# Optimization experiments

Measured on AMD Instinct MI355X. Metric: run time of the kernel, lower is better.

## Reference

```python
import jax, jax.numpy as jnp
import numpy as np
import math

IN_F, OUT_F, GRID = 1024, 1024, 7
BATCH, SEQ = 4, 4096


def _l2norm(v, eps=1e-12):
    return v / (jnp.linalg.norm(v) + eps)


def setup_inputs() -> dict:
    key = jax.random.key(0)
    k0, k1, k2, k3 = jax.random.split(key, 4)
    x = jax.random.normal(k0, (BATCH, SEQ, IN_F), dtype=jnp.float32)
    # spectral-normed base linear (weights nonzero for a meaningful baseline)
    base_w = jax.random.normal(k1, (OUT_F, IN_F), dtype=jnp.float32) * 0.02
    base_b = jnp.zeros((OUT_F,), dtype=jnp.float32)
    u = jax.random.normal(k2, (OUT_F,), dtype=jnp.float32)  # power-iteration buffer
    # Chebyshev translation points and fixed logspace scales (as in __init__)
    steps = jnp.arange(GRID, dtype=jnp.float32)
    translation = (-jnp.cos((2.0 * steps + 1.0) / (2.0 * GRID) * math.pi) * 1.5).reshape(1, 1, GRID)
    scale = (1.0 * jnp.logspace(-0.5, 0.5, GRID)).reshape(1, 1, GRID).astype(jnp.float32)
    wavelet_w = jax.random.normal(k3, (OUT_F, IN_F * GRID), dtype=jnp.float32) * 0.01
    soft_threshold = jnp.array([0.005], dtype=jnp.float32)
    output_scale = jnp.array([1.0], dtype=jnp.float32)
    return dict(x=x, base_w=base_w, base_b=base_b, u=u, translation=translation,
                scale=scale, wavelet_w=wavelet_w, soft_threshold=soft_threshold,
                output_scale=output_scale)


def reference(x, base_w, base_b, u, translation, scale, wavelet_w, soft_threshold, output_scale):
    x_flat = x.reshape(-1, x.shape[-1])  # [N, IN]
    # spectral norm: one power iteration (no grad through u, v), sigma = u' W v
    v = jax.lax.stop_gradient(_l2norm(base_w.T @ u))
    u2 = jax.lax.stop_gradient(_l2norm(base_w @ v))
    sigma = u2 @ (base_w @ v)
    w_sn = base_w / sigma
    base_out = jax.nn.silu(x_flat) @ w_sn.T + base_b  # [N, OUT]
    # wavelet (Ricker) basis expansion
    safe_scale = jnp.maximum(jnp.abs(scale), 0.1)  # [1,1,G]
    x_norm = jnp.tanh(x_flat) * 2.5  # [N, IN]
    xe = (x_norm[:, :, None] - translation) / safe_scale  # [N, IN, G]
    basis = (1.0 - xe * xe) * jnp.exp(-0.5 * xe * xe)
    kan = basis.reshape(x_flat.shape[0], -1) @ wavelet_w.T  # [N, OUT]
    thr = jax.nn.softplus(soft_threshold)
    kan = jnp.sign(kan) * jax.nn.relu(jnp.abs(kan) - thr)
    out = (base_out + kan) * output_scale
    return out.reshape(*x.shape[:-1], wavelet_w.shape[0])
```

## Files before the change

kernel.cpp:

```cpp
#include <hip/hip_runtime.h>
#include <math.h>


typedef __attribute__((ext_vector_type(4))) float  f32x4;
typedef __attribute__((ext_vector_type(8))) __bf16 bf16x8;
typedef __attribute__((ext_vector_type(8))) unsigned short u16x8;

#define NROWS 16384
#define INF   1024
#define OUTF  1024
#define GG    7
#define KKAN  7168
#define KTOT  8192

static __device__ __forceinline__ unsigned short f2bf(float f) {
  union { float f; unsigned int u; } v; v.f = f;
  unsigned int r = v.u + 0x7fffu + ((v.u >> 16) & 1u);
  return (unsigned short)(r >> 16);
}

__global__ void zero_t(float* __restrict__ t) { t[threadIdx.x] = 0.f; }

__global__ void wtu_acc(const float* __restrict__ W, const float* __restrict__ u,
                        float* __restrict__ t) {
  int tid = threadIdx.x;
  int j4 = tid * 4;
  int i0 = blockIdx.x * 16;
  f32x4 acc = {0.f, 0.f, 0.f, 0.f};
  for (int i = i0; i < i0 + 16; ++i) {
    float ui = u[i];
    f32x4 w4 = *(const f32x4*)(W + (size_t)i * INF + j4);
    acc[0] += w4[0] * ui; acc[1] += w4[1] * ui;
    acc[2] += w4[2] * ui; acc[3] += w4[3] * ui;
  }
  atomicAdd(&t[j4 + 0], acc[0]);
  atomicAdd(&t[j4 + 1], acc[1]);
  atomicAdd(&t[j4 + 2], acc[2]);
  atomicAdd(&t[j4 + 3], acc[3]);
}

__global__ void mv_w_t(const float* __restrict__ W, const float* __restrict__ t,
                       float* __restrict__ s) {
  int i = blockIdx.x;
  int tid = threadIdx.x;
  float p = 0.f;
  for (int j = tid; j < INF; j += 256) p += W[(size_t)i * INF + j] * t[j];
  __shared__ float red[256];
  red[tid] = p; __syncthreads();
  for (int k = 128; k > 0; k >>= 1) { if (tid < k) red[tid] += red[tid + k]; __syncthreads(); }
  if (tid == 0) s[i] = red[0];
}

__global__ void sigma_finish(const float* __restrict__ t, const float* __restrict__ s,
                             const float* __restrict__ st, const float* __restrict__ os,
                             float* __restrict__ scal) {
  __shared__ float r1[256], r2[256];
  int tid = threadIdx.x;
  float p1 = 0.f, p2 = 0.f;
  for (int i = tid; i < 1024; i += 256) { float a = t[i]; p1 += a * a; float b = s[i]; p2 += b * b; }
  r1[tid] = p1; r2[tid] = p2; __syncthreads();
  for (int k = 128; k > 0; k >>= 1) { if (tid < k) { r1[tid] += r1[tid + k]; r2[tid] += r2[tid + k]; } __syncthreads(); }
  if (tid == 0) {
    float nt = sqrtf(r1[0]);
    float ns = sqrtf(r2[0]);
    float nq = ns / (nt + 1e-12f);
    float sigma = nq * nq / (nq + 1e-12f);
    scal[0] = 1.f / sigma;
    scal[1] = log1pf(__expf(st[0]));
    scal[2] = os[0];
  }
}

__global__ void wsn_cast(const float* __restrict__ w, const float* __restrict__ scal,
                         unsigned short* __restrict__ Wp) {
  float is = scal[0];
  int idx = blockIdx.x * 256 + threadIdx.x;
  int row = idx >> 7, i0 = (idx & 127) << 3;
  const f32x4* p = (const f32x4*)(w + (size_t)row * INF + i0);
  f32x4 a = p[0], b = p[1];
  u16x8 v;
  v[0] = f2bf(a[0] * is); v[1] = f2bf(a[1] * is); v[2] = f2bf(a[2] * is); v[3] = f2bf(a[3] * is);
  v[4] = f2bf(b[0] * is); v[5] = f2bf(b[1] * is); v[6] = f2bf(b[2] * is); v[7] = f2bf(b[3] * is);
  *(u16x8*)(Wp + (size_t)row * KTOT + KKAN + i0) = v;
}

__global__ void wkan_cast(const float* __restrict__ w, unsigned short* __restrict__ Wp) {
  __shared__ float row[KKAN];
  int orow = blockIdx.x;
  const float* src = w + (size_t)orow * KKAN;
  for (int c = threadIdx.x * 4; c < KKAN; c += 1024)
    *(f32x4*)&row[c] = *(const f32x4*)&src[c];
  __syncthreads();
  unsigned short* dst = Wp + (size_t)orow * KTOT;
  for (int r = threadIdx.x; r < 896; r += 256) {
    int g = r >> 7, i0 = (r & 127) << 3;
    u16x8 v;
#pragma unroll
    for (int j = 0; j < 8; j++) v[j] = f2bf(row[(i0 + j) * GG + g]);
    *(u16x8*)(dst + g * 1024 + i0) = v;
  }
}

__global__ void expand_kernel(const float* __restrict__ x,
                              const float* __restrict__ translation,
                              const float* __restrict__ scale,
                              unsigned short* __restrict__ Ap,
                              int row0, int nrows) {
  float tr[GG], iss[GG];
#pragma unroll
  for (int g = 0; g < GG; g++) {
    tr[g] = translation[g];
    float s = fabsf(scale[g]);
    iss[g] = 1.f / (s < 0.1f ? 0.1f : s);
  }
  int units = nrows * (INF / 8);
  int stride = gridDim.x * blockDim.x;
  for (int uu = blockIdx.x * blockDim.x + threadIdx.x; uu < units; uu += stride) {
    int nloc = uu >> 7;
    int i0 = (uu & 127) << 3;
    const f32x4* xp = (const f32x4*)(x + (size_t)(row0 + nloc) * INF + i0);
    f32x4 xa = xp[0], xb = xp[1];
    float xv[8] = {xa[0], xa[1], xa[2], xa[3], xb[0], xb[1], xb[2], xb[3]};
    u16x8 sb, kb[GG];
#pragma unroll
    for (int j = 0; j < 8; j++) {
      float xx = xv[j];
      float si = xx / (1.f + __expf(-xx));
      sb[j] = f2bf(si);
      float e2 = __expf(2.f * xx);
      float xn = 2.5f * (1.f - 2.f / (e2 + 1.f));
#pragma unroll
      for (int g = 0; g < GG; g++) {
        float xe = (xn - tr[g]) * iss[g];
        float t2 = xe * xe;
        float b = (1.f - t2) * __expf(-0.5f * t2);
        kb[g][j] = f2bf(b);
      }
    }
    unsigned short* rp = Ap + (size_t)nloc * KTOT;
    *(u16x8*)(rp + KKAN + i0) = sb;
#pragma unroll
    for (int g = 0; g < GG; g++) *(u16x8*)(rp + g * 1024 + i0) = kb[g];
  }
}

static __device__ __forceinline__ void gload16(const unsigned short* g, unsigned short* l) {
  __builtin_amdgcn_global_load_lds(
      (const __attribute__((address_space(1))) unsigned int*)g,
      (__attribute__((address_space(3))) unsigned int*)l, 16, 0, 0);
}

#define SCB   __builtin_amdgcn_sched_barrier(0)
#define SBAR  do { SCB; __builtin_amdgcn_s_barrier(); } while (0)
#define VM(N) asm volatile("s_waitcnt vmcnt(" #N ")" ::: "memory")
#define LG(N) asm volatile("s_waitcnt lgkmcnt(" #N ")" ::: "memory")

#define STAGE(db, tt) do { \
    const unsigned short* _sa = gA + (size_t)(tt) * 64; \
    const unsigned short* _sb = gB + (size_t)(tt) * 64; \
    unsigned short* _da = ldsS + (db) * 24576; \
    unsigned short* _db = ldsS + (db) * 24576 + 16384; \
    gload16(_sa,                       _da); \
    gload16(_sa + (size_t)64  * KTOT,  _da + 4096); \
    gload16(_sa + (size_t)128 * KTOT,  _da + 8192); \
    gload16(_sa + (size_t)192 * KTOT,  _da + 12288); \
    gload16(_sb,                       _db); \
    gload16(_sb + (size_t)64  * KTOT,  _db + 4096); \
  } while (0)

#define RD8(FA, FB, bb, kx) do { \
    _Pragma("unroll") for (int i = 0; i < 4; ++i) \
      FA[i] = *(const bf16x8*)(pA + (bb) * 49152 + i * 2048 + (kx)); \
    _Pragma("unroll") for (int j = 0; j < 4; ++j) \
      FB[j] = *(const bf16x8*)(pB + (bb) * 49152 + j * 2048 + (kx)); \
  } while (0)

#define MM16(FA, FB) do { _Pragma("unroll") for (int i = 0; i < 4; ++i) \
    _Pragma("unroll") for (int j = 0; j < 4; ++j) \
      acc[i][j] = __builtin_amdgcn_mfma_f32_16x16x32_bf16(FA[i], FB[j], acc[i][j], 0, 0, 0); } while (0)

#define TILE(tt, bb, nb, db, SS, NR, W1) do { \
    RD8(fYA, fYB, bb, kx1); \
    SCB; \
    if (SS) STAGE(db, (tt) + 2); \
    SCB; \
    __builtin_amdgcn_s_setprio(1); MM16(fXA, fXB); __builtin_amdgcn_s_setprio(0); \
    LG(0); SCB; \
    W1; \
    SBAR; \
    if (NR) { RD8(fXA, fXB, nb, kx0); SCB; } \
    __builtin_amdgcn_s_setprio(1); MM16(fYA, fYB); __builtin_amdgcn_s_setprio(0); \
    LG(0); SCB; \
  } while (0)

__global__ __launch_bounds__(512, 2) void gemm_k(
    const unsigned short* __restrict__ A,
    const unsigned short* __restrict__ W,
    const float* __restrict__ bias,
    const float* __restrict__ scal,
    float* __restrict__ out) {
  __shared__ unsigned short lds[73728];

  int bid = blockIdx.x;
  int cpx = gridDim.x >> 3;
  int swz = (bid & 7) * cpx + (bid >> 3);
  int m0 = (swz >> 3) * 256;
  int n0 = (swz & 7) * 128;
  int tid = threadIdx.x;
  int wv = tid >> 6, l = tid & 63;
  int wr = wv >> 1, wc = wv & 1;

  float thr = scal[1], osc = scal[2];

  int rowq = tid >> 3;
  int swk = ((tid & 7) ^ (rowq & 7)) << 3;
  const unsigned short* gA = A + (size_t)(m0 + rowq) * KTOT + swk;
  const unsigned short* gB = W + (size_t)(n0 + rowq) * KTOT + swk;
  unsigned short* ldsS = lds + wv * 512;

  int lr = l & 15;
  int kb = (l >> 4) << 4;
  int xr = (l & 7) << 4;
  int kx0 = kb ^ xr;
  int kx1 = (64 | kb) ^ xr;
  const char* pA = (const char*)lds + (wr * 64 + lr) * 128;
  const char* pB = (const char*)lds + 32768 + (wc * 64 + lr) * 128;

  bf16x8 fXA[4], fXB[4], fYA[4], fYB[4];
  f32x4 acc[4][4] = {};

  STAGE(0, 0);
  STAGE(1, 1);
  VM(6);
  SBAR;
  RD8(fXA, fXB, 0, kx0);
  LG(0); SCB;

  for (int t = 0; t < 108; t += 3) {
    TILE(t,     0, 1, 2, 1, 1, VM(6));
    TILE(t + 1, 1, 2, 0, 1, 1, VM(6));
    TILE(t + 2, 2, 0, 1, 1, 1, VM(6));
  }
  TILE(108, 0, 1, 2, 1, 1, VM(6));
  TILE(109, 1, 2, 0, 1, 1, VM(6));
  TILE(110, 2, 0, 1, 1, 1, VM(6));
  TILE(111, 0, 1, 2, 1, 1, VM(6));

#pragma unroll
  for (int i = 0; i < 4; ++i)
#pragma unroll
    for (int j = 0; j < 4; ++j)
#pragma unroll
      for (int e = 0; e < 4; ++e) {
        float v = acc[i][j][e];
        float a = fabsf(v) - thr;
        a = a > 0.f ? a : 0.f;
        acc[i][j][e] = v > 0.f ? a : -a;
      }

  for (int t = 112; t < 124; t += 3) {
    TILE(t,     1, 2, 0, 1, 1, VM(6));
    TILE(t + 1, 2, 0, 1, 1, 1, VM(6));
    TILE(t + 2, 0, 1, 2, 1, 1, VM(6));
  }
  TILE(124, 1, 2, 0, 1, 1, VM(6));
  TILE(125, 2, 0, 1, 1, 1, VM(6));
  TILE(126, 0, 1, 2, 0, 1, VM(0));
  TILE(127, 1, 2, 0, 0, 0, (void)0);

  int rr = m0 + wr * 64 + ((l >> 4) << 2);
  int cc = n0 + wc * 64 + lr;
#pragma unroll
  for (int i = 0; i < 4; ++i)
#pragma unroll
    for (int j = 0; j < 4; ++j) {
      int c = cc + j * 16;
      float bc = bias[c];
#pragma unroll
      for (int e = 0; e < 4; ++e) {
        int r = rr + i * 16 + e;
        out[(size_t)r * OUTF + c] = (acc[i][j][e] + bc) * osc;
      }
    }
}

extern "C" void kernel_launch(void* const* d_in, const int* in_sizes, int n_in,
                              void* d_out, int out_size, void* d_ws, size_t ws_size,
                              hipStream_t stream) {
  const float* x              = (const float*)d_in[0];
  const float* base_w         = (const float*)d_in[1];
  const float* base_b         = (const float*)d_in[2];
  const float* u              = (const float*)d_in[3];
  const float* translation    = (const float*)d_in[4];
  const float* scale          = (const float*)d_in[5];
  const float* wavelet_w      = (const float*)d_in[6];
  const float* soft_threshold = (const float*)d_in[7];
  const float* output_scale   = (const float*)d_in[8];
  float* out = (float*)d_out;

  char* ws = (char*)d_ws;
  float* t_vec = (float*)ws;
  float* s_vec = t_vec + 1024;
  float* scal  = s_vec + 1024;
  unsigned short* Wp = (unsigned short*)(ws + 16384);
  char* dynbuf = ws + 16384 + (size_t)KTOT * OUTF * 2;

  size_t fixed = 16384 + (size_t)KTOT * OUTF * 2;
  size_t avail = ws_size > fixed ? ws_size - fixed : 0;

  zero_t<<<1, 1024, 0, stream>>>(t_vec);
  wtu_acc<<<64, 256, 0, stream>>>(base_w, u, t_vec);
  mv_w_t<<<1024, 256, 0, stream>>>(base_w, t_vec, s_vec);
  sigma_finish<<<1, 256, 0, stream>>>(t_vec, s_vec, soft_threshold, output_scale, scal);
  wsn_cast<<<512, 256, 0, stream>>>(base_w, scal, Wp);
  wkan_cast<<<1024, 256, 0, stream>>>(wavelet_w, Wp);

  const size_t ROW = (size_t)KTOT * 2;
  size_t total = (size_t)NROWS * ROW;
  int nch = (int)((total + (avail > 0 ? avail : 1) - 1) / (avail > 0 ? avail : 1));
  if (nch < 1) nch = 1;
  long mc = (((NROWS + nch - 1) / nch) + 255) & ~255L;
  while (mc > 256 && (size_t)mc * ROW > avail) mc -= 256;
  if (mc < 256) mc = 256;

  unsigned short* Ap = (unsigned short*)dynbuf;

  for (long r0 = 0; r0 < NROWS; r0 += mc) {
    long nr = (NROWS - r0 < mc) ? (NROWS - r0) : mc;
    expand_kernel<<<2048, 256, 0, stream>>>(x, translation, scale, Ap, (int)r0, (int)nr);
    int mt = (int)(nr / 256);
    gemm_k<<<mt * 8, 512, 0, stream>>>(Ap, Wp, base_b, scal, out + (size_t)r0 * OUTF);
  }
}
```

Before: 334.1 us.

## Deepen GEMM prefetch to three tiles and read full K-tile fragments at once

Restructures the bf16 MFMA main loop so each tile loads both K-halves of its A/B fragments from LDS in one pass and runs 32 MFMAs per tile instead of two 16-MFMA half-steps. Global staging now runs three tiles ahead across the three LDS buffers, with one barrier per tile instead of per half-step. The aim is fewer barriers and more slack to hide global-load latency. In exchange, the fragment register sets double in size, which under the 512-thread, 2-blocks-per-CU launch bound risks register spills or scheduling stalls.

New measurement: 336.9 us. Within noise of the previous version (+0.8%).

```diff
diff --git a/kernel.cpp b/kernel.cpp
--- a/kernel.cpp
+++ b/kernel.cpp
@@ -168,30 +168,39 @@
     gload16(_sb + (size_t)64  * KTOT,  _db + 4096); \
   } while (0)
 
-#define RD8(FA, FB, bb, kx) do { \
+#define RD16(FA, FB, bb) do { \
+    _Pragma("unroll") for (int i = 0; i < 4; ++i) { \
+      FA[i]     = *(const bf16x8*)(pA + (bb) * 49152 + i * 2048 + kx0); \
+      FA[4 + i] = *(const bf16x8*)(pA + (bb) * 49152 + i * 2048 + kx1); \
+    } \
+    _Pragma("unroll") for (int j = 0; j < 4; ++j) { \
+      FB[j]     = *(const bf16x8*)(pB + (bb) * 49152 + j * 2048 + kx0); \
+      FB[4 + j] = *(const bf16x8*)(pB + (bb) * 49152 + j * 2048 + kx1); \
+    } \
+  } while (0)
+
+#define MM32(FA, FB) do { \
     _Pragma("unroll") for (int i = 0; i < 4; ++i) \
-      FA[i] = *(const bf16x8*)(pA + (bb) * 49152 + i * 2048 + (kx)); \
     _Pragma("unroll") for (int j = 0; j < 4; ++j) \
-      FB[j] = *(const bf16x8*)(pB + (bb) * 49152 + j * 2048 + (kx)); \
+      acc[i][j] = __builtin_amdgcn_mfma_f32_16x16x32_bf16(FA[i], FB[j], acc[i][j], 0, 0, 0); \
+    _Pragma("unroll") for (int i = 0; i < 4; ++i) \
+    _Pragma("unroll") for (int j = 0; j < 4; ++j) \
+      acc[i][j] = __builtin_amdgcn_mfma_f32_16x16x32_bf16(FA[4 + i], FB[4 + j], acc[i][j], 0, 0, 0); \
   } while (0)
 
-#define MM16(FA, FB) do { _Pragma("unroll") for (int i = 0; i < 4; ++i) \
-    _Pragma("unroll") for (int j = 0; j < 4; ++j) \
-      acc[i][j] = __builtin_amdgcn_mfma_f32_16x16x32_bf16(FA[i], FB[j], acc[i][j], 0, 0, 0); } while (0)
-
-#define TILE(tt, bb, nb, db, SS, NR, W1) do { \
-    RD8(fYA, fYB, bb, kx1); \
+#define TILE(tt, rb, sb, SS, RA, RB, MA, MB, WAIT) do { \
+    RD16(RA, RB, rb); \
     SCB; \
-    if (SS) STAGE(db, (tt) + 2); \
+    if (SS) STAGE(sb, (tt) + 3); \
     SCB; \
-    __builtin_amdgcn_s_setprio(1); MM16(fXA, fXB); __builtin_amdgcn_s_setprio(0); \
+    __builtin_amdgcn_s_setprio(1); MM32(MA, MB); __builtin_amdgcn_s_setprio(0); \
     LG(0); SCB; \
-    W1; \
+    WAIT; \
     SBAR; \
-    if (NR) { RD8(fXA, fXB, nb, kx0); SCB; } \
-    __builtin_amdgcn_s_setprio(1); MM16(fYA, fYB); __builtin_amdgcn_s_setprio(0); \
-    LG(0); SCB; \
   } while (0)
+
+#define TILEX(tt, rb, sb, SS, WAIT) TILE(tt, rb, sb, SS, fYA, fYB, fXA, fXB, WAIT)
+#define TILEY(tt, rb, sb, SS, WAIT) TILE(tt, rb, sb, SS, fXA, fXB, fYA, fYB, WAIT)
 
 __global__ __launch_bounds__(512, 2) void gemm_k(
     const unsigned short* __restrict__ A,
@@ -226,25 +235,30 @@
   const char* pA = (const char*)lds + (wr * 64 + lr) * 128;
   const char* pB = (const char*)lds + 32768 + (wc * 64 + lr) * 128;
 
-  bf16x8 fXA[4], fXB[4], fYA[4], fYB[4];
+  bf16x8 fXA[8], fXB[8], fYA[8], fYB[8];
   f32x4 acc[4][4] = {};
 
   STAGE(0, 0);
   STAGE(1, 1);
+  STAGE(2, 2);
   VM(6);
   SBAR;
-  RD8(fXA, fXB, 0, kx0);
+  RD16(fXA, fXB, 0);
   LG(0); SCB;
-
-  for (int t = 0; t < 108; t += 3) {
-    TILE(t,     0, 1, 2, 1, 1, VM(6));
-    TILE(t + 1, 1, 2, 0, 1, 1, VM(6));
-    TILE(t + 2, 2, 0, 1, 1, 1, VM(6));
-  }
-  TILE(108, 0, 1, 2, 1, 1, VM(6));
-  TILE(109, 1, 2, 0, 1, 1, VM(6));
-  TILE(110, 2, 0, 1, 1, 1, VM(6));
-  TILE(111, 0, 1, 2, 1, 1, VM(6));
+  SBAR;
+
+  for (int t = 0; t < 108; t += 6) {
+    TILEX(t,     1, 0, 1, VM(6));
+    TILEY(t + 1, 2, 1, 1, VM(6));
+    TILEX(t + 2, 0, 2, 1, VM(6));
+    TILEY(t + 3, 1, 0, 1, VM(6));
+    TILEX(t + 4, 2, 1, 1, VM(6));
+    TILEY(t + 5, 0, 2, 1, VM(6));
+  }
+  TILEX(108, 1, 0, 1, VM(6));
+  TILEY(109, 2, 1, 1, VM(6));
+  TILEX(110, 0, 2, 1, VM(6));
+  TILEY(111, 1, 0, 1, VM(6));
 
 #pragma unroll
   for (int i = 0; i < 4; ++i)
@@ -258,15 +272,22 @@
         acc[i][j][e] = v > 0.f ? a : -a;
       }
 
-  for (int t = 112; t < 124; t += 3) {
-    TILE(t,     1, 2, 0, 1, 1, VM(6));
-    TILE(t + 1, 2, 0, 1, 1, 1, VM(6));
-    TILE(t + 2, 0, 1, 2, 1, 1, VM(6));
-  }
-  TILE(124, 1, 2, 0, 1, 1, VM(6));
-  TILE(125, 2, 0, 1, 1, 1, VM(6));
-  TILE(126, 0, 1, 2, 0, 1, VM(0));
-  TILE(127, 1, 2, 0, 0, 0, (void)0);
+  TILEX(112, 2, 1, 1, VM(6));
+  TILEY(113, 0, 2, 1, VM(6));
+  TILEX(114, 1, 0, 1, VM(6));
+  TILEY(115, 2, 1, 1, VM(6));
+  TILEX(116, 0, 2, 1, VM(6));
+  TILEY(117, 1, 0, 1, VM(6));
+  TILEX(118, 2, 1, 1, VM(6));
+  TILEY(119, 0, 2, 1, VM(6));
+  TILEX(120, 1, 0, 1, VM(6));
+  TILEY(121, 2, 1, 1, VM(6));
+  TILEX(122, 0, 2, 1, VM(6));
+  TILEY(123, 1, 0, 1, VM(6));
+  TILEX(124, 2, 1, 1, VM(6));
+  TILEY(125, 0, 0, 0, VM(0));
+  TILEX(126, 1, 0, 0, (void)0);
+  __builtin_amdgcn_s_setprio(1); MM32(fYA, fYB); __builtin_amdgcn_s_setprio(0);
 
   int rr = m0 + wr * 64 + ((l >> 4) << 2);
   int cc = n0 + wc * 64 + lr;
```

## Halve GEMM block to 4 waves, each computing a 128x64 output tile

Applied to the files above, without the earlier changes.

The GEMM block keeps its 256x128 output tile but now runs 256 threads (4 waves) instead of 512 (8 waves). Each wave computes a 128x64 sub-tile with 8x4 MFMA accumulators, so each B fragment read from LDS is reused across twice as many MFMAs. Staging loops are rescaled to 8 A-row and 4 B-row global-to-LDS loads per thread, with matching vmcnt waits. The cost is much higher register pressure and only one wave per SIMD, which leaves less room to hide LDS and memory latency.

After: 373.7 us. 1.12x slower.

```diff
diff --git a/kernel.cpp b/kernel.cpp
--- a/kernel.cpp
+++ b/kernel.cpp
@@ -159,41 +159,39 @@
     const unsigned short* _sa = gA + (size_t)(tt) * 64; \
     const unsigned short* _sb = gB + (size_t)(tt) * 64; \
     unsigned short* _da = ldsS + (db) * 24576; \
-    unsigned short* _db = ldsS + (db) * 24576 + 16384; \
-    gload16(_sa,                       _da); \
-    gload16(_sa + (size_t)64  * KTOT,  _da + 4096); \
-    gload16(_sa + (size_t)128 * KTOT,  _da + 8192); \
-    gload16(_sa + (size_t)192 * KTOT,  _da + 12288); \
-    gload16(_sb,                       _db); \
-    gload16(_sb + (size_t)64  * KTOT,  _db + 4096); \
+    unsigned short* _db2 = ldsS + (db) * 24576 + 16384; \
+    _Pragma("unroll") for (int r = 0; r < 8; ++r) \
+      gload16(_sa + (size_t)(r * 32) * KTOT, _da + r * 2048); \
+    _Pragma("unroll") for (int r = 0; r < 4; ++r) \
+      gload16(_sb + (size_t)(r * 32) * KTOT, _db2 + r * 2048); \
   } while (0)
 
-#define RD8(FA, FB, bb, kx) do { \
-    _Pragma("unroll") for (int i = 0; i < 4; ++i) \
+#define RD12(FA, FB, bb, kx) do { \
+    _Pragma("unroll") for (int i = 0; i < 8; ++i) \
       FA[i] = *(const bf16x8*)(pA + (bb) * 49152 + i * 2048 + (kx)); \
     _Pragma("unroll") for (int j = 0; j < 4; ++j) \
       FB[j] = *(const bf16x8*)(pB + (bb) * 49152 + j * 2048 + (kx)); \
   } while (0)
 
-#define MM16(FA, FB) do { _Pragma("unroll") for (int i = 0; i < 4; ++i) \
+#define MM32h(FA, FB) do { _Pragma("unroll") for (int i = 0; i < 8; ++i) \
     _Pragma("unroll") for (int j = 0; j < 4; ++j) \
       acc[i][j] = __builtin_amdgcn_mfma_f32_16x16x32_bf16(FA[i], FB[j], acc[i][j], 0, 0, 0); } while (0)
 
 #define TILE(tt, bb, nb, db, SS, NR, W1) do { \
-    RD8(fYA, fYB, bb, kx1); \
+    RD12(fYA, fYB, bb, kx1); \
     SCB; \
     if (SS) STAGE(db, (tt) + 2); \
     SCB; \
-    __builtin_amdgcn_s_setprio(1); MM16(fXA, fXB); __builtin_amdgcn_s_setprio(0); \
+    __builtin_amdgcn_s_setprio(1); MM32h(fXA, fXB); __builtin_amdgcn_s_setprio(0); \
     LG(0); SCB; \
     W1; \
     SBAR; \
-    if (NR) { RD8(fXA, fXB, nb, kx0); SCB; } \
-    __builtin_amdgcn_s_setprio(1); MM16(fYA, fYB); __builtin_amdgcn_s_setprio(0); \
+    if (NR) { RD12(fXA, fXB, nb, kx0); SCB; } \
+    __builtin_amdgcn_s_setprio(1); MM32h(fYA, fYB); __builtin_amdgcn_s_setprio(0); \
     LG(0); SCB; \
   } while (0)
 
-__global__ __launch_bounds__(512, 2) void gemm_k(
+__global__ __launch_bounds__(256, 1) void gemm_k(
     const unsigned short* __restrict__ A,
     const unsigned short* __restrict__ W,
     const float* __restrict__ bias,
@@ -223,31 +221,31 @@
   int xr = (l & 7) << 4;
   int kx0 = kb ^ xr;
   int kx1 = (64 | kb) ^ xr;
-  const char* pA = (const char*)lds + (wr * 64 + lr) * 128;
+  const char* pA = (const char*)lds + (wr * 128 + lr) * 128;
   const char* pB = (const char*)lds + 32768 + (wc * 64 + lr) * 128;
 
-  bf16x8 fXA[4], fXB[4], fYA[4], fYB[4];
-  f32x4 acc[4][4] = {};
+  bf16x8 fXA[8], fXB[4], fYA[8], fYB[4];
+  f32x4 acc[8][4] = {};
 
   STAGE(0, 0);
   STAGE(1, 1);
-  VM(6);
+  VM(12);
   SBAR;
-  RD8(fXA, fXB, 0, kx0);
+  RD12(fXA, fXB, 0, kx0);
   LG(0); SCB;
 
   for (int t = 0; t < 108; t += 3) {
-    TILE(t,     0, 1, 2, 1, 1, VM(6));
-    TILE(t + 1, 1, 2, 0, 1, 1, VM(6));
-    TILE(t + 2, 2, 0, 1, 1, 1, VM(6));
-  }
-  TILE(108, 0, 1, 2, 1, 1, VM(6));
-  TILE(109, 1, 2, 0, 1, 1, VM(6));
-  TILE(110, 2, 0, 1, 1, 1, VM(6));
-  TILE(111, 0, 1, 2, 1, 1, VM(6));
-
-#pragma unroll
-  for (int i = 0; i < 4; ++i)
+    TILE(t,     0, 1, 2, 1, 1, VM(12));
+    TILE(t + 1, 1, 2, 0, 1, 1, VM(12));
+    TILE(t + 2, 2, 0, 1, 1, 1, VM(12));
+  }
+  TILE(108, 0, 1, 2, 1, 1, VM(12));
+  TILE(109, 1, 2, 0, 1, 1, VM(12));
+  TILE(110, 2, 0, 1, 1, 1, VM(12));
+  TILE(111, 0, 1, 2, 1, 1, VM(12));
+
+#pragma unroll
+  for (int i = 0; i < 8; ++i)
 #pragma unroll
     for (int j = 0; j < 4; ++j)
 #pragma unroll
@@ -258,20 +256,27 @@
         acc[i][j][e] = v > 0.f ? a : -a;
       }
 
-  for (int t = 112; t < 124; t += 3) {
-    TILE(t,     1, 2, 0, 1, 1, VM(6));
-    TILE(t + 1, 2, 0, 1, 1, 1, VM(6));
-    TILE(t + 2, 0, 1, 2, 1, 1, VM(6));
-  }
-  TILE(124, 1, 2, 0, 1, 1, VM(6));
-  TILE(125, 2, 0, 1, 1, 1, VM(6));
+  TILE(112, 1, 2, 0, 1, 1, VM(12));
+  TILE(113, 2, 0, 1, 1, 1, VM(12));
+  TILE(114, 0, 1, 2, 1, 1, VM(12));
+  TILE(115, 1, 2, 0, 1, 1, VM(12));
+  TILE(116, 2, 0, 1, 1, 1, VM(12));
+  TILE(117, 0, 1, 2, 1, 1, VM(12));
+  TILE(118, 1, 2, 0, 1, 1, VM(12));
+  TILE(119, 2, 0, 1, 1, 1, VM(12));
+  TILE(120, 0, 1, 2, 1, 1, VM(12));
+  TILE(121, 1, 2, 0, 1, 1, VM(12));
+  TILE(122, 2, 0, 1, 1, 1, VM(12));
+  TILE(123, 0, 1, 2, 1, 1, VM(12));
+  TILE(124, 1, 2, 0, 1, 1, VM(12));
+  TILE(125, 2, 0, 1, 1, 1, VM(12));
   TILE(126, 0, 1, 2, 0, 1, VM(0));
   TILE(127, 1, 2, 0, 0, 0, (void)0);
 
-  int rr = m0 + wr * 64 + ((l >> 4) << 2);
+  int rr = m0 + wr * 128 + ((l >> 4) << 2);
   int cc = n0 + wc * 64 + lr;
 #pragma unroll
-  for (int i = 0; i < 4; ++i)
+  for (int i = 0; i < 8; ++i)
 #pragma unroll
     for (int j = 0; j < 4; ++j) {
       int c = cc + j * 16;
@@ -329,6 +334,6 @@
     long nr = (NROWS - r0 < mc) ? (NROWS - r0) : mc;
     expand_kernel<<<2048, 256, 0, stream>>>(x, translation, scale, Ap, (int)r0, (int)nr);
     int mt = (int)(nr / 256);
-    gemm_k<<<mt * 8, 512, 0, stream>>>(Ap, Wp, base_b, scal, out + (size_t)r0 * OUTF);
-  }
-}
+    gemm_k<<<mt * 8, 256, 0, stream>>>(Ap, Wp, base_b, scal, out + (size_t)r0 * OUTF);
+  }
+}
```

## Fuse Ricker basis expansion into GEMM A-tile generation

Applied to the files above, without the earlier changes.

Removes the materialized 16384x8192 bf16 expanded activation matrix. A prep kernel now writes only bf16 silu(x) and fp32 tanh-normalized x. The GEMM computes the seven wavelet basis values per K tile in registers and writes them into LDS instead of loading A tiles from global memory. The wavelet weights are reordered into a matching (i-chunk, g) interleaved layout. This trades much HBM traffic for per-tile exp work in the GEMM main loop, which may compete with MFMA issue and raise register pressure.

New measurement: 506.4 us. +51.6%, slower.

```diff
diff --git a/kernel.cpp b/kernel.cpp
--- a/kernel.cpp
+++ b/kernel.cpp
@@ -5,6 +5,7 @@
 typedef __attribute__((ext_vector_type(4))) float  f32x4;
 typedef __attribute__((ext_vector_type(8))) __bf16 bf16x8;
 typedef __attribute__((ext_vector_type(8))) unsigned short u16x8;
+typedef __attribute__((ext_vector_type(4))) unsigned int u32x4;
 
 #define NROWS 16384
 #define INF   1024
@@ -97,31 +98,23 @@
     u16x8 v;
 #pragma unroll
     for (int j = 0; j < 8; j++) v[j] = f2bf(row[(i0 + j) * GG + g]);
-    *(u16x8*)(dst + g * 1024 + i0) = v;
-  }
-}
-
-__global__ void expand_kernel(const float* __restrict__ x,
-                              const float* __restrict__ translation,
-                              const float* __restrict__ scale,
-                              unsigned short* __restrict__ Ap,
-                              int row0, int nrows) {
-  float tr[GG], iss[GG];
-#pragma unroll
-  for (int g = 0; g < GG; g++) {
-    tr[g] = translation[g];
-    float s = fabsf(scale[g]);
-    iss[g] = 1.f / (s < 0.1f ? 0.1f : s);
-  }
-  int units = nrows * (INF / 8);
+    *(u16x8*)(dst + ((i0 >> 6) * 7 + g) * 64 + (i0 & 63)) = v;
+  }
+}
+
+__global__ void xs_prep(const float* __restrict__ x,
+                        unsigned short* __restrict__ siluP,
+                        float* __restrict__ xnP) {
+  int units = NROWS * (INF / 8);
   int stride = gridDim.x * blockDim.x;
   for (int uu = blockIdx.x * blockDim.x + threadIdx.x; uu < units; uu += stride) {
-    int nloc = uu >> 7;
+    int row = uu >> 7;
     int i0 = (uu & 127) << 3;
-    const f32x4* xp = (const f32x4*)(x + (size_t)(row0 + nloc) * INF + i0);
+    const f32x4* xp = (const f32x4*)(x + (size_t)row * INF + i0);
     f32x4 xa = xp[0], xb = xp[1];
     float xv[8] = {xa[0], xa[1], xa[2], xa[3], xb[0], xb[1], xb[2], xb[3]};
-    u16x8 sb, kb[GG];
+    u16x8 sb;
+    f32x4 na, nb;
 #pragma unroll
     for (int j = 0; j < 8; j++) {
       float xx = xv[j];
@@ -129,18 +122,12 @@
       sb[j] = f2bf(si);
       float e2 = __expf(2.f * xx);
       float xn = 2.5f * (1.f - 2.f / (e2 + 1.f));
-#pragma unroll
-      for (int g = 0; g < GG; g++) {
-        float xe = (xn - tr[g]) * iss[g];
-        float t2 = xe * xe;
-        float b = (1.f - t2) * __expf(-0.5f * t2);
-        kb[g][j] = f2bf(b);
-      }
+      if (j < 4) na[j] = xn; else nb[j - 4] = xn;
     }
-    unsigned short* rp = Ap + (size_t)nloc * KTOT;
-    *(u16x8*)(rp + KKAN + i0) = sb;
-#pragma unroll
-    for (int g = 0; g < GG; g++) *(u16x8*)(rp + g * 1024 + i0) = kb[g];
+    *(u16x8*)(siluP + (size_t)row * INF + i0) = sb;
+    float* np = xnP + (size_t)row * INF + i0;
+    *(f32x4*)np = na;
+    *(f32x4*)(np + 4) = nb;
   }
 }
 
@@ -150,22 +137,61 @@
       (__attribute__((address_space(3))) unsigned int*)l, 16, 0, 0);
 }
 
+static __device__ __forceinline__ float basisf(float x, float is_, float ntri) {
+  float xe = fmaf(x, is_, ntri);
+  float t2 = xe * xe;
+  float ex = __expf(-0.5f * t2);
+  return (1.f - t2) * ex;
+}
+
 #define SCB   __builtin_amdgcn_sched_barrier(0)
 #define SBAR  do { SCB; __builtin_amdgcn_s_barrier(); } while (0)
 #define VM(N) asm volatile("s_waitcnt vmcnt(" #N ")" ::: "memory")
 #define LG(N) asm volatile("s_waitcnt lgkmcnt(" #N ")" ::: "memory")
 
-#define STAGE(db, tt) do { \
-    const unsigned short* _sa = gA + (size_t)(tt) * 64; \
-    const unsigned short* _sb = gB + (size_t)(tt) * 64; \
+#define XLOAD(ic) do { \
+    const f32x4* xp_ = (const f32x4*)(xnp + (size_t)(m0 + xrow) * 1024 + (ic) * 64 + 32 * xh); \
+    _Pragma("unroll") for (int q = 0; q < 8; ++q) xd[q] = xp_[q]; \
+  } while (0)
+
+#define BGLOAD(db, t2) do { \
+    const unsigned short* _sb = gB + (size_t)(t2) * 64; \
+    unsigned short* _db2 = ldsS + (db) * 24576 + 16384; \
+    gload16(_sb, _db2); \
+    gload16(_sb + (size_t)64 * KTOT, _db2 + 4096); \
+  } while (0)
+
+#define CW(db, t2) do { \
+    int g2s = (t2) % 7; \
+    float is_ = ldsF[g2s]; \
+    float ntri = ldsF[7 + g2s]; \
+    char* wp_ = (char*)lds + (db) * 49152 + xrow * 128; \
+    _Pragma("unroll") for (int q = 0; q < 4; ++q) { \
+      unsigned int ov0, ov1, ov2, ov3; \
+      { f32x4 xv = xd[2 * q]; \
+        float b0 = basisf(xv[0], is_, ntri), b1 = basisf(xv[1], is_, ntri); \
+        float b2 = basisf(xv[2], is_, ntri), b3 = basisf(xv[3], is_, ntri); \
+        asm("v_cvt_pk_bf16_f32 %0, %1, %2" : "=v"(ov0) : "v"(b0), "v"(b1)); \
+        asm("v_cvt_pk_bf16_f32 %0, %1, %2" : "=v"(ov1) : "v"(b2), "v"(b3)); } \
+      { f32x4 xv = xd[2 * q + 1]; \
+        float b0 = basisf(xv[0], is_, ntri), b1 = basisf(xv[1], is_, ntri); \
+        float b2 = basisf(xv[2], is_, ntri), b3 = basisf(xv[3], is_, ntri); \
+        asm("v_cvt_pk_bf16_f32 %0, %1, %2" : "=v"(ov2) : "v"(b0), "v"(b1)); \
+        asm("v_cvt_pk_bf16_f32 %0, %1, %2" : "=v"(ov3) : "v"(b2), "v"(b3)); } \
+      u32x4 w4 = {ov0, ov1, ov2, ov3}; \
+      *(u32x4*)(wp_ + (((4 * xh + q) ^ (xrow & 7)) << 4)) = w4; \
+    } \
+  } while (0)
+
+#define STAGE_BASE(db, t2) do { \
+    const unsigned short* _sa = gS + (size_t)((t2) - 112) * 64; \
+    const unsigned short* _sb = gB + (size_t)(t2) * 64; \
     unsigned short* _da = ldsS + (db) * 24576; \
-    unsigned short* _db = ldsS + (db) * 24576 + 16384; \
-    gload16(_sa,                       _da); \
-    gload16(_sa + (size_t)64  * KTOT,  _da + 4096); \
-    gload16(_sa + (size_t)128 * KTOT,  _da + 8192); \
-    gload16(_sa + (size_t)192 * KTOT,  _da + 12288); \
-    gload16(_sb,                       _db); \
-    gload16(_sb + (size_t)64  * KTOT,  _db + 4096); \
+    unsigned short* _db2 = _da + 16384; \
+    _Pragma("unroll") for (int r = 0; r < 4; ++r) \
+      gload16(_sa + (size_t)(r * 64) * 1024, _da + r * 4096); \
+    _Pragma("unroll") for (int r = 0; r < 2; ++r) \
+      gload16(_sb + (size_t)(r * 64) * KTOT, _db2 + r * 4096); \
   } while (0)
 
 #define RD8(FA, FB, bb, kx) do { \
@@ -179,10 +205,28 @@
     _Pragma("unroll") for (int j = 0; j < 4; ++j) \
       acc[i][j] = __builtin_amdgcn_mfma_f32_16x16x32_bf16(FA[i], FB[j], acc[i][j], 0, 0, 0); } while (0)
 
-#define TILE(tt, bb, nb, db, SS, NR, W1) do { \
+#define TILE_K(tt, bb, nb, db, W1) do { \
     RD8(fYA, fYB, bb, kx1); \
     SCB; \
-    if (SS) STAGE(db, (tt) + 2); \
+    { int t2_ = (tt) + 2; int g2_ = t2_ % 7; int ic_ = t2_ / 7; \
+      if (g2_ == 0) { XLOAD(ic_); } \
+      SCB; \
+      BGLOAD(db, t2_); \
+      SCB; \
+      __builtin_amdgcn_s_setprio(1); MM16(fXA, fXB); __builtin_amdgcn_s_setprio(0); \
+      CW(db, t2_); } \
+    LG(0); SCB; \
+    W1; \
+    SBAR; \
+    RD8(fXA, fXB, nb, kx0); SCB; \
+    __builtin_amdgcn_s_setprio(1); MM16(fYA, fYB); __builtin_amdgcn_s_setprio(0); \
+    LG(0); SCB; \
+  } while (0)
+
+#define TILE_B(tt, bb, nb, db, SS, NR, W1) do { \
+    RD8(fYA, fYB, bb, kx1); \
+    SCB; \
+    if (SS) STAGE_BASE(db, (tt) + 2); \
     SCB; \
     __builtin_amdgcn_s_setprio(1); MM16(fXA, fXB); __builtin_amdgcn_s_setprio(0); \
     LG(0); SCB; \
@@ -194,12 +238,16 @@
   } while (0)
 
 __global__ __launch_bounds__(512, 2) void gemm_k(
-    const unsigned short* __restrict__ A,
+    const float* __restrict__ xnp,
+    const unsigned short* __restrict__ silu,
     const unsigned short* __restrict__ W,
     const float* __restrict__ bias,
     const float* __restrict__ scal,
+    const float* __restrict__ trP,
+    const float* __restrict__ scP,
     float* __restrict__ out) {
-  __shared__ unsigned short lds[73728];
+  __shared__ unsigned short lds[73760];
+  float* ldsF = (float*)(lds + 73728);
 
   int bid = blockIdx.x;
   int cpx = gridDim.x >> 3;
@@ -214,9 +262,12 @@
 
   int rowq = tid >> 3;
   int swk = ((tid & 7) ^ (rowq & 7)) << 3;
-  const unsigned short* gA = A + (size_t)(m0 + rowq) * KTOT + swk;
   const unsigned short* gB = W + (size_t)(n0 + rowq) * KTOT + swk;
+  const unsigned short* gS = silu + (size_t)(m0 + rowq) * 1024 + swk;
   unsigned short* ldsS = lds + wv * 512;
+
+  int xrow = tid >> 1;
+  int xh = tid & 1;
 
   int lr = l & 15;
   int kb = (l >> 4) << 4;
@@ -227,24 +278,41 @@
   const char* pB = (const char*)lds + 32768 + (wc * 64 + lr) * 128;
 
   bf16x8 fXA[4], fXB[4], fYA[4], fYB[4];
+  f32x4 xd[8];
   f32x4 acc[4][4] = {};
 
-  STAGE(0, 0);
-  STAGE(1, 1);
-  VM(6);
+  if (tid < 7) {
+    float s = fabsf(scP[tid]);
+    s = s < 0.1f ? 0.1f : s;
+    float is_ = 1.0f / s;
+    ldsF[tid] = is_;
+    ldsF[7 + tid] = -trP[tid] * is_;
+  }
+  SBAR;
+
+  XLOAD(0);
+  SCB;
+  BGLOAD(0, 0);
+  SCB;
+  CW(0, 0);
+  BGLOAD(1, 1);
+  SCB;
+  CW(1, 1);
+  LG(0);
+  VM(2);
   SBAR;
   RD8(fXA, fXB, 0, kx0);
   LG(0); SCB;
 
   for (int t = 0; t < 108; t += 3) {
-    TILE(t,     0, 1, 2, 1, 1, VM(6));
-    TILE(t + 1, 1, 2, 0, 1, 1, VM(6));
-    TILE(t + 2, 2, 0, 1, 1, 1, VM(6));
-  }
-  TILE(108, 0, 1, 2, 1, 1, VM(6));
-  TILE(109, 1, 2, 0, 1, 1, VM(6));
-  TILE(110, 2, 0, 1, 1, 1, VM(6));
-  TILE(111, 0, 1, 2, 1, 1, VM(6));
+    TILE_K(t,     0, 1, 2, VM(2));
+    TILE_K(t + 1, 1, 2, 0, VM(2));
+    TILE_K(t + 2, 2, 0, 1, VM(2));
+  }
+  TILE_K(108, 0, 1, 2, VM(2));
+  TILE_K(109, 1, 2, 0, VM(2));
+  TILE_B(110, 2, 0, 1, 1, 1, VM(6));
+  TILE_B(111, 0, 1, 2, 1, 1, VM(6));
 
 #pragma unroll
   for (int i = 0; i < 4; ++i)
@@ -258,15 +326,22 @@
         acc[i][j][e] = v > 0.f ? a : -a;
       }
 
-  for (int t = 112; t < 124; t += 3) {
-    TILE(t,     1, 2, 0, 1, 1, VM(6));
-    TILE(t + 1, 2, 0, 1, 1, 1, VM(6));
-    TILE(t + 2, 0, 1, 2, 1, 1, VM(6));
-  }
-  TILE(124, 1, 2, 0, 1, 1, VM(6));
-  TILE(125, 2, 0, 1, 1, 1, VM(6));
-  TILE(126, 0, 1, 2, 0, 1, VM(0));
-  TILE(127, 1, 2, 0, 0, 0, (void)0);
+  TILE_B(112, 1, 2, 0, 1, 1, VM(6));
+  TILE_B(113, 2, 0, 1, 1, 1, VM(6));
+  TILE_B(114, 0, 1, 2, 1, 1, VM(6));
+  TILE_B(115, 1, 2, 0, 1, 1, VM(6));
+  TILE_B(116, 2, 0, 1, 1, 1, VM(6));
+  TILE_B(117, 0, 1, 2, 1, 1, VM(6));
+  TILE_B(118, 1, 2, 0, 1, 1, VM(6));
+  TILE_B(119, 2, 0, 1, 1, 1, VM(6));
+  TILE_B(120, 0, 1, 2, 1, 1, VM(6));
+  TILE_B(121, 1, 2, 0, 1, 1, VM(6));
+  TILE_B(122, 2, 0, 1, 1, 1, VM(6));
+  TILE_B(123, 0, 1, 2, 1, 1, VM(6));
+  TILE_B(124, 1, 2, 0, 1, 1, VM(6));
+  TILE_B(125, 2, 0, 1, 1, 1, VM(6));
+  TILE_B(126, 0, 1, 2, 0, 1, VM(0));
+  TILE_B(127, 1, 2, 0, 0, 0, (void)0);
 
   int rr = m0 + wr * 64 + ((l >> 4) << 2);
   int cc = n0 + wc * 64 + lr;
@@ -302,11 +377,9 @@
   float* t_vec = (float*)ws;
   float* s_vec = t_vec + 1024;
   float* scal  = s_vec + 1024;
-  unsigned short* Wp = (unsigned short*)(ws + 16384);
-  char* dynbuf = ws + 16384 + (size_t)KTOT * OUTF * 2;
-
-  size_t fixed = 16384 + (size_t)KTOT * OUTF * 2;
-  size_t avail = ws_size > fixed ? ws_size - fixed : 0;
+  unsigned short* Wp    = (unsigned short*)(ws + 16384);
+  unsigned short* siluP = (unsigned short*)(ws + 16384 + (size_t)KTOT * OUTF * 2);
+  float* xnP = (float*)(ws + 16384 + (size_t)KTOT * OUTF * 2 + (size_t)NROWS * INF * 2);
 
   zero_t<<<1, 1024, 0, stream>>>(t_vec);
   wtu_acc<<<64, 256, 0, stream>>>(base_w, u, t_vec);
@@ -314,21 +387,8 @@
   sigma_finish<<<1, 256, 0, stream>>>(t_vec, s_vec, soft_threshold, output_scale, scal);
   wsn_cast<<<512, 256, 0, stream>>>(base_w, scal, Wp);
   wkan_cast<<<1024, 256, 0, stream>>>(wavelet_w, Wp);
-
-  const size_t ROW = (size_t)KTOT * 2;
-  size_t total = (size_t)NROWS * ROW;
-  int nch = (int)((total + (avail > 0 ? avail : 1) - 1) / (avail > 0 ? avail : 1));
-  if (nch < 1) nch = 1;
-  long mc = (((NROWS + nch - 1) / nch) + 255) & ~255L;
-  while (mc > 256 && (size_t)mc * ROW > avail) mc -= 256;
-  if (mc < 256) mc = 256;
-
-  unsigned short* Ap = (unsigned short*)dynbuf;
-
-  for (long r0 = 0; r0 < NROWS; r0 += mc) {
-    long nr = (NROWS - r0 < mc) ? (NROWS - r0) : mc;
-    expand_kernel<<<2048, 256, 0, stream>>>(x, translation, scale, Ap, (int)r0, (int)nr);
-    int mt = (int)(nr / 256);
-    gemm_k<<<mt * 8, 512, 0, stream>>>(Ap, Wp, base_b, scal, out + (size_t)r0 * OUTF);
-  }
-}
+  xs_prep<<<2048, 256, 0, stream>>>(x, siluP, xnP);
+
+  gemm_k<<<(NROWS / 256) * 8, 512, 0, stream>>>(xnP, siluP, Wp, base_b, scal,
+                                                translation, scale, out);
+}
```
